# Kernel optimization log

Measured on AMD Instinct MI355X. Metric: run time of the kernel, lower is better.

## Reference

```python
import jax, jax.numpy as jnp
import numpy as np

B, TQ, TV = 4, 256, 256
H, D, U = 512, 512, 256  # hidden_size, value_size, units


def setup_inputs() -> dict:
    key = jax.random.key(0)
    ks = jax.random.split(key, 8)
    s = 0.02
    return {
        "query": jax.random.normal(ks[0], (B, TQ, H), dtype=jnp.float32),
        "values": jax.random.normal(ks[1], (B, TV, D), dtype=jnp.float32),
        "W1": jax.random.normal(ks[2], (H, U), dtype=jnp.float32) * s,
        "b1": jnp.zeros((U,), dtype=jnp.float32),
        "W2": jax.random.normal(ks[3], (D, U), dtype=jnp.float32) * s,
        "b2": jnp.zeros((U,), dtype=jnp.float32),
        "V": jax.random.normal(ks[4], (U, 1), dtype=jnp.float32) * s,
        "bV": jnp.zeros((1,), dtype=jnp.float32),
    }


def reference(query, values, W1, b1, W2, b2, V, bV):
    # query: [B,Tq,H]  values: [B,Tv,D]
    q = jnp.einsum("bqh,hu->bqu", query, W1) + b1          # [B,Tq,U]
    v = jnp.einsum("bvd,du->bvu", values, W2) + b2          # [B,Tv,U]
    # tf.repeat over Tq is just a broadcast of v; same math without materializing repeats twice
    hidden = jnp.tanh(q[:, :, None, :] + v[:, None, :, :])  # [B,Tq,Tv,U]
    score = jnp.einsum("bqvu,u->bqv", hidden, V[:, 0]) + bV[0]  # [B,Tq,Tv]
    attn = jax.nn.softmax(score, axis=2)                    # softmax over Tv (axis=2 of score)
    context = jnp.einsum("bqv,bvd->bqd", attn, values)      # [B,Tq,D]
    return context, attn[..., None]                          # weights returned as [B,Tq,Tv,1] like TF
```

## Files before the change

kernel.cpp:

```cpp
#include <hip/hip_runtime.h>
#include <math.h>


typedef float f4 __attribute__((ext_vector_type(4)));
typedef float f2 __attribute__((ext_vector_type(2)));

#define B_    4
#define TQ_   256
#define TV_   256
#define D_    512
#define U_    256
#define KDIM  512
#define MROWS 1024
#define BKP   32
#define KQ    128
#define NSTEP (KQ / BKP)

#define C2LOG2E 2.8853900817779268f

#define PELEMS  262144
#define EQ_OFF  (8 * PELEMS)
#define EVT_OFF (9 * PELEMS)

#if __has_builtin(__builtin_amdgcn_exp2f)
#define EXP2F(x) __builtin_amdgcn_exp2f(x)
#else
#define EXP2F(x) exp2f(x)
#endif
#if __has_builtin(__builtin_amdgcn_rcpf)
#define RCPF(x) __builtin_amdgcn_rcpf(x)
#else
#define RCPF(x) (1.0f / (x))
#endif

__global__ __launch_bounds__(256) void proj_partial(
    const float* __restrict__ query, const float* __restrict__ values,
    const float* __restrict__ W1, const float* __restrict__ W2,
    float* __restrict__ ws)
{
    const int proj = blockIdx.z;
    const int ks   = blockIdx.y;
    const int tile = blockIdx.x;

    __shared__ __align__(16) float As[BKP][68];
    __shared__ __align__(16) float Bs[BKP][68];

    const int tid = threadIdx.x;
    const int tx = tid & 15, ty = tid >> 4;
    const int trow = tid >> 2, tk = (tid & 3) * 8;
    const int dk = tid >> 3, dcol = (tid & 7) * 8;
    const int kb = ks * KQ;

    int m0, n0;
    const float* Tsrc;
    const float* Dsrc;
    if (proj == 0) {
        m0 = (tile >> 2) * 64;  n0 = (tile & 3) * 64;
        Tsrc = query  + (size_t)(m0 + trow) * KDIM + kb + tk;
        Dsrc = W1     + (size_t)(kb + dk) * U_ + n0 + dcol;
    } else {
        m0 = (tile & 3) * 64;   n0 = (tile >> 2) * 64;
        Tsrc = values + (size_t)(n0 + trow) * KDIM + kb + tk;
        Dsrc = W2     + (size_t)(kb + dk) * U_ + m0 + dcol;
    }

    f4 t0 = *(const f4*)(Tsrc);
    f4 t1 = *(const f4*)(Tsrc + 4);
    f4 d0 = *(const f4*)(Dsrc);
    f4 d1 = *(const f4*)(Dsrc + 4);

    float acc[4][4] = {};

    for (int s = 0; s < NSTEP; ++s) {
        __syncthreads();
        if (proj == 0) {
            #pragma unroll
            for (int j = 0; j < 4; ++j) {
                As[tk + j][trow]     = t0[j];
                As[tk + 4 + j][trow] = t1[j];
            }
            *(f4*)&Bs[dk][dcol]     = d0;
            *(f4*)&Bs[dk][dcol + 4] = d1;
        } else {
            #pragma unroll
            for (int j = 0; j < 4; ++j) {
                Bs[tk + j][trow]     = t0[j];
                Bs[tk + 4 + j][trow] = t1[j];
            }
            *(f4*)&As[dk][dcol]     = d0;
            *(f4*)&As[dk][dcol + 4] = d1;
        }
        __syncthreads();

        if (s + 1 < NSTEP) {
            const float* Tn = Tsrc + (s + 1) * BKP;
            const float* Dn = Dsrc + (size_t)(s + 1) * BKP * U_;
            t0 = *(const f4*)(Tn);
            t1 = *(const f4*)(Tn + 4);
            d0 = *(const f4*)(Dn);
            d1 = *(const f4*)(Dn + 4);
        }

        #pragma unroll
        for (int kk = 0; kk < BKP; ++kk) {
            f4 av = *(const f4*)&As[kk][ty * 4];
            f4 bv = *(const f4*)&Bs[kk][tx * 4];
            #pragma unroll
            for (int i = 0; i < 4; ++i)
                #pragma unroll
                for (int j = 0; j < 4; ++j)
                    acc[i][j] = fmaf(av[i], bv[j], acc[i][j]);
        }
    }

    const int cstride = proj ? MROWS : U_;
    float* P = ws + (size_t)(proj * 4 + ks) * PELEMS;
    #pragma unroll
    for (int i = 0; i < 4; ++i) {
        f4 o = {acc[i][0], acc[i][1], acc[i][2], acc[i][3]};
        *(f4*)&P[(size_t)(m0 + ty * 4 + i) * cstride + n0 + tx * 4] = o;
    }
}

__global__ __launch_bounds__(256) void proj_combine(
    const float* __restrict__ b1, const float* __restrict__ b2,
    float* __restrict__ ws)
{
    const int g = blockIdx.x * 256 + threadIdx.x;
    const int proj = g >> 16;
    const int rem  = g & 65535;
    f4* wsf4 = (f4*)ws;

    f4 p = wsf4[(size_t)(proj * 4)     * 65536 + rem];
    p   += wsf4[(size_t)(proj * 4 + 1) * 65536 + rem];
    p   += wsf4[(size_t)(proj * 4 + 2) * 65536 + rem];
    p   += wsf4[(size_t)(proj * 4 + 3) * 65536 + rem];

    f4 bias;
    if (proj == 0) {
        bias = ((const f4*)b1)[rem & 63];
    } else {
        float bb = b2[rem >> 8];
        bias = f4{bb, bb, bb, bb};
    }

    f4 e;
    #pragma unroll
    for (int j = 0; j < 4; ++j)
        e[j] = EXP2F((p[j] + bias[j]) * C2LOG2E);

    wsf4[(size_t)(8 + proj) * 65536 + rem] = e;
}

__global__ __launch_bounds__(256) void score_softmax(
    const float* __restrict__ Vw, const float* __restrict__ ws,
    float* __restrict__ out)
{
    __shared__ __align__(16) f4 epk[U_];
    __shared__ float redmin[4][2];
    __shared__ float redsum[4][2];

    const int tid = threadIdx.x;
    const int b  = blockIdx.y;
    const int q0 = blockIdx.x * 2;

    {
        const float* eqr = ws + EQ_OFF + (size_t)(b * TQ_ + q0) * U_;
        epk[tid] = f4{eqr[tid], eqr[U_ + tid], Vw[tid], 0.0f};
    }

    const float* evp = ws + EVT_OFF + (size_t)b * TV_ + tid;

    float evA[8], evB[8];
    #pragma unroll
    for (int i = 0; i < 8; ++i) evA[i] = evp[(size_t)i * MROWS];

    __syncthreads();

    float p0 = 0.f, p1 = 0.f;

    #define SGRP(BUF, G)                                                 \
        _Pragma("unroll")                                                \
        for (int i = 0; i < 8; ++i) {                                    \
            f4 t = epk[(G) * 8 + i];                                     \
            float d0 = fmaf(t.x, BUF[i], 1.0f);                          \
            float d1 = fmaf(t.y, BUF[i], 1.0f);                          \
            p0 = fmaf(t.z, RCPF(d0), p0);                                \
            p1 = fmaf(t.z, RCPF(d1), p1);                                \
        }

    #pragma unroll
    for (int g = 0; g < 32; g += 2) {
        #pragma unroll
        for (int i = 0; i < 8; ++i)
            evB[i] = evp[(size_t)((g + 1) * 8 + i) * MROWS];
        SGRP(evA, g)
        if (g + 2 < 32) {
            #pragma unroll
            for (int i = 0; i < 8; ++i)
                evA[i] = evp[(size_t)((g + 2) * 8 + i) * MROWS];
        }
        SGRP(evB, g + 1)
    }
    #undef SGRP

    const int w = tid >> 6, lane = tid & 63;
    float m0 = p0, m1 = p1;
    #pragma unroll
    for (int off = 32; off; off >>= 1) {
        m0 = fminf(m0, __shfl_xor(m0, off));
        m1 = fminf(m1, __shfl_xor(m1, off));
    }
    if (lane == 0) { redmin[w][0] = m0; redmin[w][1] = m1; }
    __syncthreads();
    m0 = fminf(fminf(redmin[0][0], redmin[1][0]), fminf(redmin[2][0], redmin[3][0]));
    m1 = fminf(fminf(redmin[0][1], redmin[1][1]), fminf(redmin[2][1], redmin[3][1]));

    float e0 = EXP2F((m0 - p0) * C2LOG2E);
    float e1 = EXP2F((m1 - p1) * C2LOG2E);

    float s0 = e0, s1 = e1;
    #pragma unroll
    for (int off = 32; off; off >>= 1) {
        s0 += __shfl_xor(s0, off);
        s1 += __shfl_xor(s1, off);
    }
    if (lane == 0) { redsum[w][0] = s0; redsum[w][1] = s1; }
    __syncthreads();
    s0 = redsum[0][0] + redsum[1][0] + redsum[2][0] + redsum[3][0];
    s1 = redsum[0][1] + redsum[1][1] + redsum[2][1] + redsum[3][1];

    float* attn = out + (size_t)B_ * TQ_ * D_ + (size_t)(b * TQ_ + q0) * TV_;
    attn[tid]       = e0 * (1.0f / s0);
    attn[TV_ + tid] = e1 * (1.0f / s1);
}

__global__ __launch_bounds__(256) void context_gemm(
    const float* __restrict__ values, float* __restrict__ out)
{
    __shared__ __align__(16) f4 apk[TV_];

    const int tid = threadIdx.x;
    const int b  = blockIdx.y;
    const int q0 = blockIdx.x * 4;

    const float* at = out + (size_t)B_ * TQ_ * D_ + (size_t)(b * TQ_ + q0) * TV_;
    apk[tid] = f4{at[tid], at[TV_ + tid], at[2 * TV_ + tid], at[3 * TV_ + tid]};

    const f2* vp = (const f2*)(values + (size_t)b * TV_ * D_) + tid;

    f2 bufA[8], bufB[8];
    #pragma unroll
    for (int i = 0; i < 8; ++i) bufA[i] = vp[(size_t)i * (D_ / 2)];

    __syncthreads();

    f2 acc0 = {0.f, 0.f}, acc1 = {0.f, 0.f}, acc2 = {0.f, 0.f}, acc3 = {0.f, 0.f};

    #define CGRP(BUF, G)                                                 \
        _Pragma("unroll")                                                \
        for (int i = 0; i < 8; ++i) {                                    \
            f4 a = apk[(G) * 8 + i];                                     \
            f2 val = BUF[i];                                             \
            acc0 += a.x * val;                                           \
            acc1 += a.y * val;                                           \
            acc2 += a.z * val;                                           \
            acc3 += a.w * val;                                           \
        }

    #pragma unroll
    for (int g = 0; g < 32; g += 2) {
        #pragma unroll
        for (int i = 0; i < 8; ++i)
            bufB[i] = vp[(size_t)((g + 1) * 8 + i) * (D_ / 2)];
        CGRP(bufA, g)
        if (g + 2 < 32) {
            #pragma unroll
            for (int i = 0; i < 8; ++i)
                bufA[i] = vp[(size_t)((g + 2) * 8 + i) * (D_ / 2)];
        }
        CGRP(bufB, g + 1)
    }
    #undef CGRP

    float* orow = out + (size_t)(b * TQ_ + q0) * D_ + 2 * tid;
    *(f2*)(orow)          = acc0;
    *(f2*)(orow + D_)     = acc1;
    *(f2*)(orow + 2 * D_) = acc2;
    *(f2*)(orow + 3 * D_) = acc3;
}

extern "C" void kernel_launch(void* const* d_in, const int* in_sizes, int n_in,
                              void* d_out, int out_size, void* d_ws, size_t ws_size,
                              hipStream_t stream) {
    const float* query  = (const float*)d_in[0];
    const float* values = (const float*)d_in[1];
    const float* W1     = (const float*)d_in[2];
    const float* b1     = (const float*)d_in[3];
    const float* W2     = (const float*)d_in[4];
    const float* b2     = (const float*)d_in[5];
    const float* Vw     = (const float*)d_in[6];
    float* out = (float*)d_out;
    float* ws  = (float*)d_ws;

    proj_partial<<<dim3(64, 4, 2), 256, 0, stream>>>(query, values, W1, W2, ws);
    proj_combine<<<dim3(512), 256, 0, stream>>>(b1, b2, ws);
    score_softmax<<<dim3(TQ_ / 2, B_), 256, 0, stream>>>(Vw, ws, out);
    context_gemm<<<dim3(TQ_ / 4, B_), 256, 0, stream>>>(values, out);
}
```

Baseline: 44.07 us.

## Replace split-K fp32 projection GEMMs with bf16 MFMA kernel and fused epilogue

The two projection GEMMs move from a split-K fp32 FMA kernel plus a separate combine kernel to a single bf16 MFMA kernel (16x16x32) that runs the full K loop with double-buffered LDS. The bias add and exp2 epilogue are fused in, so one kernel launch and the partial-sum round trip through workspace go away. The trade-off is bf16 rounding of inputs and weights, which could hurt accuracy, and fewer blocks (128 instead of 512), which lowers parallelism. The epilogue also writes scalars with a strided layout instead of vector stores.

```diff
diff --git a/kernel.cpp b/kernel.cpp
--- a/kernel.cpp
+++ b/kernel.cpp
@@ -4,6 +4,8 @@
 
 typedef float f4 __attribute__((ext_vector_type(4)));
 typedef float f2 __attribute__((ext_vector_type(2)));
+typedef __attribute__((ext_vector_type(8))) short s8v;
+typedef __attribute__((ext_vector_type(8))) unsigned short u8v;
 
 #define B_    4
 #define TQ_   256
@@ -12,15 +14,11 @@
 #define U_    256
 #define KDIM  512
 #define MROWS 1024
-#define BKP   32
-#define KQ    128
-#define NSTEP (KQ / BKP)
 
 #define C2LOG2E 2.8853900817779268f
 
-#define PELEMS  262144
-#define EQ_OFF  (8 * PELEMS)
-#define EVT_OFF (9 * PELEMS)
+#define EQ_OFF  0
+#define EVT_OFF 262144
 
 #if __has_builtin(__builtin_amdgcn_exp2f)
 #define EXP2F(x) __builtin_amdgcn_exp2f(x)
@@ -33,123 +31,123 @@
 #define RCPF(x) (1.0f / (x))
 #endif
 
-__global__ __launch_bounds__(256) void proj_partial(
+__device__ __forceinline__ unsigned short f2bf(float f) {
+    union { float f; unsigned u; } v; v.f = f;
+    return (unsigned short)((v.u + 0x7FFF + ((v.u >> 16) & 1)) >> 16);
+}
+
+__global__ __launch_bounds__(256) void proj_mfma(
     const float* __restrict__ query, const float* __restrict__ values,
-    const float* __restrict__ W1, const float* __restrict__ W2,
+    const float* __restrict__ W1, const float* __restrict__ b1,
+    const float* __restrict__ W2, const float* __restrict__ b2,
     float* __restrict__ ws)
 {
-    const int proj = blockIdx.z;
-    const int ks   = blockIdx.y;
-    const int tile = blockIdx.x;
-
-    __shared__ __align__(16) float As[BKP][68];
-    __shared__ __align__(16) float Bs[BKP][68];
-
-    const int tid = threadIdx.x;
-    const int tx = tid & 15, ty = tid >> 4;
-    const int trow = tid >> 2, tk = (tid & 3) * 8;
-    const int dk = tid >> 3, dcol = (tid & 7) * 8;
-    const int kb = ks * KQ;
+    __shared__ unsigned short Al[2][64][40];
+    __shared__ unsigned short Bl[2][64][40];
+
+    const int tid  = threadIdx.x;
+    const int proj = blockIdx.y;
+    const int x    = blockIdx.x;
 
     int m0, n0;
-    const float* Tsrc;
-    const float* Dsrc;
+    if (proj == 0) { m0 = (x >> 2) * 64; n0 = (x & 3) * 64; }
+    else           { m0 = (x & 3) * 64;  n0 = (x >> 2) * 64; }
+
+    const int sr = tid >> 2;
+    const int sk = (tid & 3) * 8;
+
+    const float* dptr = (proj ? values + (size_t)(n0 + sr) * KDIM
+                              : query  + (size_t)(m0 + sr) * KDIM) + sk;
+    const float* tptr = (proj ? W2 + (m0 + sr) : W1 + (n0 + sr))
+                        + (size_t)sk * U_;
+
+    f4 d0, d1;
+    float tv0, tv1, tv2, tv3, tv4, tv5, tv6, tv7;
+
+#define LOADR(S)                                                        \
+    do {                                                                \
+        const float* dp = dptr + (size_t)(S) * 32;                      \
+        d0 = *(const f4*)(dp);                                          \
+        d1 = *(const f4*)(dp + 4);                                      \
+        const float* tp = tptr + (size_t)(S) * 32 * U_;                 \
+        tv0 = tp[0];       tv1 = tp[U_];       tv2 = tp[2 * U_];        \
+        tv3 = tp[3 * U_];  tv4 = tp[4 * U_];   tv5 = tp[5 * U_];        \
+        tv6 = tp[6 * U_];  tv7 = tp[7 * U_];                            \
+    } while (0)
+
+#define WRITEB(BUF)                                                     \
+    do {                                                                \
+        u8v dd, tt;                                                     \
+        dd[0] = f2bf(d0[0]); dd[1] = f2bf(d0[1]);                       \
+        dd[2] = f2bf(d0[2]); dd[3] = f2bf(d0[3]);                       \
+        dd[4] = f2bf(d1[0]); dd[5] = f2bf(d1[1]);                       \
+        dd[6] = f2bf(d1[2]); dd[7] = f2bf(d1[3]);                       \
+        tt[0] = f2bf(tv0); tt[1] = f2bf(tv1); tt[2] = f2bf(tv2);        \
+        tt[3] = f2bf(tv3); tt[4] = f2bf(tv4); tt[5] = f2bf(tv5);        \
+        tt[6] = f2bf(tv6); tt[7] = f2bf(tv7);                           \
+        unsigned short* ddst = proj ? &Bl[BUF][sr][sk] : &Al[BUF][sr][sk]; \
+        unsigned short* tdst = proj ? &Al[BUF][sr][sk] : &Bl[BUF][sr][sk]; \
+        *(u8v*)ddst = dd;                                               \
+        *(u8v*)tdst = tt;                                               \
+    } while (0)
+
+    f4 acc0 = {}, acc1 = {}, acc2 = {}, acc3 = {};
+
+    const int w  = tid >> 6;
+    const int l  = tid & 63;
+    const int fr = l & 15;
+    const int fk = (l >> 4) * 8;
+
+    LOADR(0);
+    WRITEB(0);
+
+    for (int s = 0; s < 16; ++s) {
+        __syncthreads();
+        if (s + 1 < 16) LOADR(s + 1);
+        {
+            const int bu = s & 1;
+            s8v af  = *(const s8v*)&Al[bu][w * 16 + fr][fk];
+            s8v bf0 = *(const s8v*)&Bl[bu][fr][fk];
+            s8v bf1 = *(const s8v*)&Bl[bu][16 + fr][fk];
+            s8v bf2 = *(const s8v*)&Bl[bu][32 + fr][fk];
+            s8v bf3 = *(const s8v*)&Bl[bu][48 + fr][fk];
+            acc0 = __builtin_amdgcn_mfma_f32_16x16x32_bf16(af, bf0, acc0, 0, 0, 0);
+            acc1 = __builtin_amdgcn_mfma_f32_16x16x32_bf16(af, bf1, acc1, 0, 0, 0);
+            acc2 = __builtin_amdgcn_mfma_f32_16x16x32_bf16(af, bf2, acc2, 0, 0, 0);
+            acc3 = __builtin_amdgcn_mfma_f32_16x16x32_bf16(af, bf3, acc3, 0, 0, 0);
+        }
+        if (s + 1 < 16) WRITEB((s + 1) & 1);
+    }
+#undef LOADR
+#undef WRITEB
+
+    const int orow  = m0 + w * 16 + (l >> 4) * 4;
+    const int ocol0 = n0 + (l & 15);
+
     if (proj == 0) {
-        m0 = (tile >> 2) * 64;  n0 = (tile & 3) * 64;
-        Tsrc = query  + (size_t)(m0 + trow) * KDIM + kb + tk;
-        Dsrc = W1     + (size_t)(kb + dk) * U_ + n0 + dcol;
+        float* E = ws + EQ_OFF;
+        #pragma unroll
+        for (int nt = 0; nt < 4; ++nt) {
+            const int n = ocol0 + nt * 16;
+            const float bias = b1[n];
+            const f4 a = nt == 0 ? acc0 : nt == 1 ? acc1 : nt == 2 ? acc2 : acc3;
+            #pragma unroll
+            for (int r = 0; r < 4; ++r)
+                E[(size_t)(orow + r) * U_ + n] =
+                    EXP2F((a[r] + bias) * C2LOG2E);
+        }
     } else {
-        m0 = (tile & 3) * 64;   n0 = (tile >> 2) * 64;
-        Tsrc = values + (size_t)(n0 + trow) * KDIM + kb + tk;
-        Dsrc = W2     + (size_t)(kb + dk) * U_ + m0 + dcol;
-    }
-
-    f4 t0 = *(const f4*)(Tsrc);
-    f4 t1 = *(const f4*)(Tsrc + 4);
-    f4 d0 = *(const f4*)(Dsrc);
-    f4 d1 = *(const f4*)(Dsrc + 4);
-
-    float acc[4][4] = {};
-
-    for (int s = 0; s < NSTEP; ++s) {
-        __syncthreads();
-        if (proj == 0) {
+        float* E = ws + EVT_OFF;
+        #pragma unroll
+        for (int nt = 0; nt < 4; ++nt) {
+            const int n = ocol0 + nt * 16;
+            const f4 a = nt == 0 ? acc0 : nt == 1 ? acc1 : nt == 2 ? acc2 : acc3;
             #pragma unroll
-            for (int j = 0; j < 4; ++j) {
-                As[tk + j][trow]     = t0[j];
-                As[tk + 4 + j][trow] = t1[j];
-            }
-            *(f4*)&Bs[dk][dcol]     = d0;
-            *(f4*)&Bs[dk][dcol + 4] = d1;
-        } else {
-            #pragma unroll
-            for (int j = 0; j < 4; ++j) {
-                Bs[tk + j][trow]     = t0[j];
-                Bs[tk + 4 + j][trow] = t1[j];
-            }
-            *(f4*)&As[dk][dcol]     = d0;
-            *(f4*)&As[dk][dcol + 4] = d1;
-        }
-        __syncthreads();
-
-        if (s + 1 < NSTEP) {
-            const float* Tn = Tsrc + (s + 1) * BKP;
-            const float* Dn = Dsrc + (size_t)(s + 1) * BKP * U_;
-            t0 = *(const f4*)(Tn);
-            t1 = *(const f4*)(Tn + 4);
-            d0 = *(const f4*)(Dn);
-            d1 = *(const f4*)(Dn + 4);
-        }
-
-        #pragma unroll
-        for (int kk = 0; kk < BKP; ++kk) {
-            f4 av = *(const f4*)&As[kk][ty * 4];
-            f4 bv = *(const f4*)&Bs[kk][tx * 4];
-            #pragma unroll
-            for (int i = 0; i < 4; ++i)
-                #pragma unroll
-                for (int j = 0; j < 4; ++j)
-                    acc[i][j] = fmaf(av[i], bv[j], acc[i][j]);
-        }
-    }
-
-    const int cstride = proj ? MROWS : U_;
-    float* P = ws + (size_t)(proj * 4 + ks) * PELEMS;
-    #pragma unroll
-    for (int i = 0; i < 4; ++i) {
-        f4 o = {acc[i][0], acc[i][1], acc[i][2], acc[i][3]};
-        *(f4*)&P[(size_t)(m0 + ty * 4 + i) * cstride + n0 + tx * 4] = o;
-    }
-}
-
-__global__ __launch_bounds__(256) void proj_combine(
-    const float* __restrict__ b1, const float* __restrict__ b2,
-    float* __restrict__ ws)
-{
-    const int g = blockIdx.x * 256 + threadIdx.x;
-    const int proj = g >> 16;
-    const int rem  = g & 65535;
-    f4* wsf4 = (f4*)ws;
-
-    f4 p = wsf4[(size_t)(proj * 4)     * 65536 + rem];
-    p   += wsf4[(size_t)(proj * 4 + 1) * 65536 + rem];
-    p   += wsf4[(size_t)(proj * 4 + 2) * 65536 + rem];
-    p   += wsf4[(size_t)(proj * 4 + 3) * 65536 + rem];
-
-    f4 bias;
-    if (proj == 0) {
-        bias = ((const f4*)b1)[rem & 63];
-    } else {
-        float bb = b2[rem >> 8];
-        bias = f4{bb, bb, bb, bb};
-    }
-
-    f4 e;
-    #pragma unroll
-    for (int j = 0; j < 4; ++j)
-        e[j] = EXP2F((p[j] + bias[j]) * C2LOG2E);
-
-    wsf4[(size_t)(8 + proj) * 65536 + rem] = e;
+            for (int r = 0; r < 4; ++r)
+                E[(size_t)(orow + r) * MROWS + n] =
+                    EXP2F((a[r] + b2[orow + r]) * C2LOG2E);
+        }
+    }
 }
 
 __global__ __launch_bounds__(256) void score_softmax(
@@ -303,8 +301,7 @@
     float* out = (float*)d_out;
     float* ws  = (float*)d_ws;
 
-    proj_partial<<<dim3(64, 4, 2), 256, 0, stream>>>(query, values, W1, W2, ws);
-    proj_combine<<<dim3(512), 256, 0, stream>>>(b1, b2, ws);
+    proj_mfma<<<dim3(64, 2), 256, 0, stream>>>(query, values, W1, b1, W2, b2, ws);
     score_softmax<<<dim3(TQ_ / 2, B_), 256, 0, stream>>>(Vw, ws, out);
     context_gemm<<<dim3(TQ_ / 4, B_), 256, 0, stream>>>(values, out);
 }
```

Measured after the change: 42.24 us. 1.04x faster.
